# Performance work log

Hardware: AMD Instinct MI355X
Metric: run time of the kernel (lower is better)

The kernel has to match this reference:

```python
import jax, jax.numpy as jnp
import numpy as np

B, N, D = 4, 4096, 1024
HEADS, DIM_HEAD = 16, 64
INNER = HEADS * DIM_HEAD
LN_EPS = 1e-5


def next_fast_len(n):
    # smallest 5-smooth integer >= n (matches scipy.fftpack.next_fast_len)
    while True:
        m = n
        for p in (2, 3, 5):
            while m % p == 0:
                m //= p
        if m == 1:
            return n
        n += 1


def setup_inputs() -> dict:
    key = jax.random.key(0)
    k = jax.random.split(key, 6)
    x = jax.random.normal(k[0], (B, N, D), dtype=jnp.float32)
    gamma = jnp.ones((D,), dtype=jnp.float32)
    beta = jnp.zeros((D,), dtype=jnp.float32)
    alpha = jax.random.normal(k[1], (HEADS,), dtype=jnp.float32)
    w_in = jax.random.normal(k[2], (INNER, D), dtype=jnp.float32) * 0.02
    w_out = jax.random.normal(k[3], (D, INNER), dtype=jnp.float32) * 0.02
    return {"x": x, "gamma": gamma, "beta": beta, "alpha": alpha, "w_in": w_in, "w_out": w_out}


def reference(x, gamma, beta, alpha, w_in, w_out):
    b, n, d = x.shape
    h, dh = HEADS, DIM_HEAD
    # LayerNorm (biased variance, eps=1e-5)
    mu = jnp.mean(x, axis=-1, keepdims=True)
    var = jnp.var(x, axis=-1, keepdims=True)
    xn = (x - mu) * jax.lax.rsqrt(var + LN_EPS) * gamma + beta
    # project_in (no bias), split heads: b n (h d) -> b h n d
    xi = jnp.einsum('bnd,ed->bne', xn, w_in)
    xi = xi.reshape(b, n, h, dh).transpose(0, 2, 1, 3)  # [b,h,n,dh]
    # exponential decay weights per head: alpha * (1-alpha)**flip(arange(n)) -> [h, n]
    a = jax.nn.sigmoid(alpha)[:, None]
    weights = a * (1.0 - a) ** jnp.arange(n - 1, -1, -1, dtype=x.dtype)[None, :]
    # FFT-based causal correlation (conv1d_fft)
    fast_len = next_fast_len(n + n - 1)
    f_x = jnp.fft.rfft(xi, n=fast_len, axis=-2)           # [b,h,L',dh] complex
    f_w = jnp.fft.rfft(weights, n=fast_len, axis=-1)      # [h,L'] complex
    out = jnp.fft.irfft(f_x * jnp.conj(f_w)[None, :, :, None], fast_len, axis=-2)
    out = jnp.roll(out, -1, axis=-2)
    out = out[:, :, fast_len - n:, :]                      # last n positions -> [b,h,n,dh]
    # merge heads and project out
    out = out.transpose(0, 2, 1, 3).reshape(b, n, h * dh)
    return jnp.einsum('bne,de->bnd', out, w_out)
```

## Files before the change

### kernel.cpp

```cpp
#include <hip/hip_runtime.h>
#include <hip/hip_bf16.h>

#define B_ 4
#define N_ 4096
#define D_ 1024
#define H_ 16
#define INNER_ 1024
#define M_ (B_ * N_)
#define CH_ 128
#define CL_ 32

using bf16x8 = __attribute__((ext_vector_type(8))) __bf16;
using f32x4  = __attribute__((ext_vector_type(4))) float;

__device__ __forceinline__ float bf2f(unsigned short v) {
  return __uint_as_float(((unsigned)v) << 16);
}
__device__ __forceinline__ unsigned short f2bf(float f) {
  __hip_bfloat16 h = __float2bfloat16(f);
  return *reinterpret_cast<unsigned short*>(&h);
}
__device__ __forceinline__ float sigm(float x) { return 1.f / (1.f + expf(-x)); }

__device__ __forceinline__ void gload_lds16(const void* g, void* l) {
  __builtin_amdgcn_global_load_lds(
      (const __attribute__((address_space(1))) unsigned int*)g,
      (__attribute__((address_space(3))) unsigned int*)l, 16, 0, 0);
}

__global__ __launch_bounds__(256) void cast_bf16_kernel(
    const float* __restrict__ in, __hip_bfloat16* __restrict__ out, int n4) {
  int i = blockIdx.x * 256 + threadIdx.x;
  if (i >= n4) return;
  float4 v = reinterpret_cast<const float4*>(in)[i];
  ushort4 o;
  o.x = f2bf(v.x); o.y = f2bf(v.y); o.z = f2bf(v.z); o.w = f2bf(v.w);
  reinterpret_cast<ushort4*>(out)[i] = o;
}

__global__ __launch_bounds__(256) void ln_kernel(
    const float* __restrict__ x, const float* __restrict__ gamma,
    const float* __restrict__ beta, __hip_bfloat16* __restrict__ xn) {
  const long row = blockIdx.x;
  const int t = threadIdx.x;
  const float4 v = reinterpret_cast<const float4*>(x + row * D_)[t];
  float s = v.x + v.y + v.z + v.w;
  float s2 = v.x * v.x + v.y * v.y + v.z * v.z + v.w * v.w;
#pragma unroll
  for (int o = 32; o > 0; o >>= 1) {
    s += __shfl_down(s, o);
    s2 += __shfl_down(s2, o);
  }
  __shared__ float red[8];
  const int lane = t & 63, wv = t >> 6;
  if (lane == 0) { red[wv] = s; red[4 + wv] = s2; }
  __syncthreads();
  const float sum = red[0] + red[1] + red[2] + red[3];
  const float sum2 = red[4] + red[5] + red[6] + red[7];
  const float mu = sum * (1.f / D_);
  const float var = sum2 * (1.f / D_) - mu * mu;
  const float rs = rsqrtf(var + 1e-5f);
  const float4 g = reinterpret_cast<const float4*>(gamma)[t];
  const float4 bb = reinterpret_cast<const float4*>(beta)[t];
  ushort4 o;
  o.x = f2bf((v.x - mu) * rs * g.x + bb.x);
  o.y = f2bf((v.y - mu) * rs * g.y + bb.y);
  o.z = f2bf((v.z - mu) * rs * g.z + bb.z);
  o.w = f2bf((v.w - mu) * rs * g.w + bb.w);
  reinterpret_cast<ushort4*>(xn + row * D_)[t] = o;
}

__device__ __forceinline__ void stc(float* p, float v) { *p = v; }
__device__ __forceinline__ void stc(__hip_bfloat16* p, float v) { *p = __float2bfloat16(v); }

template <typename TOUT, int NT>
__global__ __launch_bounds__(512, 2) void gemm256_kernel(
    const __hip_bfloat16* __restrict__ A, const __hip_bfloat16* __restrict__ Bt,
    TOUT* __restrict__ C, int M, int N, int K) {
  static_assert(NT >= 4, "ring needs >=4 tiles");
  __shared__ __align__(16) char lds[131072];
  const int tid = threadIdx.x;
  const int lane = tid & 63;
  const int wave = tid >> 6;

  int wg = blockIdx.y * gridDim.x + blockIdx.x;
  wg = (wg & 7) * 32 + (wg >> 3);
  const int bx = wg & 3;
  const int by = wg >> 2;
  const long bm = (long)by * 256;
  const long bn = (long)bx * 256;

  const int u0  = (tid & 7) ^ ((tid >> 3) & 7);
  const int r0  = 2 * (tid >> 3) + (u0 >> 2);
  const int ck0 = u0 & 3;
  const __hip_bfloat16* sA0 = A  + (bm + r0) * (long)K + ck0 * 8;
  const __hip_bfloat16* sA1 = sA0 + 128l * K;
  const __hip_bfloat16* sB0 = Bt + (bn + r0) * (long)K + ck0 * 8;
  const __hip_bfloat16* sB1 = sB0 + 128l * K;
  char* dbase = (char*)lds + wave * 1024;

  const int wm = wave >> 2;
  const int wn = wave & 3;
  const int fr = lane & 15;
  const int ck = lane >> 4;
  const int pos = (((fr & 1) << 2) | ck) ^ ((fr >> 1) & 7);
  const int laneA = wm * 8192 + (fr >> 1) * 128 + pos * 16;
  const int laneB = 16384 + wn * 4096 + (fr >> 1) * 128 + pos * 16;

  f32x4 acc[8][4] = {};

#define STAGE_A(kt) do { const int _s = (kt) & 3;                         \
    gload_lds16(sA0 + (long)(kt) * 32, dbase + _s * 32768);               \
    gload_lds16(sA1 + (long)(kt) * 32, dbase + _s * 32768 + 8192); } while (0)
#define STAGE_B(kt) do { const int _s = (kt) & 3;                         \
    gload_lds16(sB0 + (long)(kt) * 32, dbase + _s * 32768 + 16384);       \
    gload_lds16(sB1 + (long)(kt) * 32, dbase + _s * 32768 + 24576); } while (0)

  STAGE_A(0); STAGE_B(0);
  STAGE_A(1); STAGE_B(1);
  asm volatile("s_waitcnt vmcnt(4)" ::: "memory");
  __builtin_amdgcn_s_barrier();
  asm volatile("" ::: "memory");

#pragma unroll 4
  for (int t = 0; t < NT; ++t) {
    const char* base = (const char*)lds + (t & 3) * 32768;
    bf16x8 bv[4], av[4];
#pragma unroll
    for (int c = 0; c < 4; ++c) bv[c] = *(const bf16x8*)(base + laneB + c * 1024);
#pragma unroll
    for (int r = 0; r < 4; ++r) av[r] = *(const bf16x8*)(base + laneA + r * 1024);
    if (t + 2 < NT) STAGE_A(t + 2);
    __builtin_amdgcn_s_setprio(1);
#pragma unroll
    for (int r = 0; r < 4; ++r)
#pragma unroll
      for (int c = 0; c < 4; ++c)
        acc[r][c] = __builtin_amdgcn_mfma_f32_16x16x32_bf16(av[r], bv[c], acc[r][c], 0, 0, 0);
    __builtin_amdgcn_s_setprio(0);
#pragma unroll
    for (int r = 0; r < 4; ++r) av[r] = *(const bf16x8*)(base + laneA + (r + 4) * 1024);
    if (t + 2 < NT) STAGE_B(t + 2);
    __builtin_amdgcn_s_setprio(1);
#pragma unroll
    for (int r = 0; r < 4; ++r)
#pragma unroll
      for (int c = 0; c < 4; ++c)
        acc[r + 4][c] = __builtin_amdgcn_mfma_f32_16x16x32_bf16(av[r], bv[c], acc[r + 4][c], 0, 0, 0);
    __builtin_amdgcn_s_setprio(0);
    if (t < NT - 3) asm volatile("s_waitcnt vmcnt(4)" ::: "memory");
    else            asm volatile("s_waitcnt vmcnt(0)" ::: "memory");
    __builtin_amdgcn_s_barrier();
    asm volatile("" ::: "memory");
  }
#undef STAGE_A
#undef STAGE_B

  const int cr = ck * 4;
#pragma unroll
  for (int rf = 0; rf < 8; ++rf)
#pragma unroll
    for (int cf = 0; cf < 4; ++cf)
#pragma unroll
      for (int r = 0; r < 4; ++r) {
        const long row = bm + wm * 128 + rf * 16 + cr + r;
        const long col = bn + wn * 64 + cf * 16 + fr;
        stc(&C[row * (long)N + col], acc[rf][cf][r]);
      }
}

__global__ __launch_bounds__(256) void scan_local_kernel(
    const __hip_bfloat16* __restrict__ xi, __hip_bfloat16* __restrict__ y,
    float* __restrict__ finals, const float* __restrict__ alpha) {
  const int e0 = threadIdx.x * 4;
  const int c = blockIdx.y;
  const int b = blockIdx.z;
  const float a = sigm(alpha[e0 >> 6]);
  const float om = 1.f - a;
  long base = ((long)b * N_ + (long)c * CL_) * INNER_ + e0;
  float y0 = 0.f, y1 = 0.f, y2 = 0.f, y3 = 0.f;
  for (int t = 0; t < CL_; ++t) {
    ushort4 u = *(const ushort4*)(xi + base);
    y0 = om * y0 + a * bf2f(u.x);
    y1 = om * y1 + a * bf2f(u.y);
    y2 = om * y2 + a * bf2f(u.z);
    y3 = om * y3 + a * bf2f(u.w);
    ushort4 o;
    o.x = f2bf(y0); o.y = f2bf(y1); o.z = f2bf(y2); o.w = f2bf(y3);
    *(ushort4*)(y + base) = o;
    base += INNER_;
  }
  float4 f4 = make_float4(y0, y1, y2, y3);
  *reinterpret_cast<float4*>(&finals[((long)b * CH_ + c) * INNER_ + e0]) = f4;
}

__global__ __launch_bounds__(256) void scan_carry_kernel(
    const float* __restrict__ finals, float* __restrict__ carries,
    const float* __restrict__ alpha) {
  const int g = blockIdx.x * 256 + threadIdx.x;
  const int b = g >> 10;
  const int e = g & 1023;
  const float a = sigm(alpha[e >> 6]);
  const float dc = powf(1.f - a, (float)CL_);
  float carry = 0.f;
  for (int c = 0; c < CH_; ++c) {
    const long idx = ((long)b * CH_ + c) * INNER_ + e;
    carries[idx] = carry;
    carry = finals[idx] + dc * carry;
  }
}

__global__ __launch_bounds__(256) void scan_fix_kernel(
    __hip_bfloat16* __restrict__ y, const float* __restrict__ carries,
    const float* __restrict__ alpha) {
  const int t = blockIdx.y;
  const int c = t >> 5;
  if (c == 0) return;
  const int tl = t & 31;
  const int e0 = threadIdx.x * 4;
  const int b = blockIdx.z;
  const float a = sigm(alpha[e0 >> 6]);
  const float om = 1.f - a;
  const float w = exp2f((float)(tl + 1) * log2f(om));
  const float4 cr = *reinterpret_cast<const float4*>(
      &carries[((long)b * CH_ + c) * INNER_ + e0]);
  const long idx = ((long)b * N_ + t) * INNER_ + e0;
  ushort4 u = *(const ushort4*)(y + idx);
  ushort4 o;
  o.x = f2bf(bf2f(u.x) + cr.x * w);
  o.y = f2bf(bf2f(u.y) + cr.y * w);
  o.z = f2bf(bf2f(u.z) + cr.z * w);
  o.w = f2bf(bf2f(u.w) + cr.w * w);
  *(ushort4*)(y + idx) = o;
}

extern "C" void kernel_launch(void* const* d_in, const int* in_sizes, int n_in,
                              void* d_out, int out_size, void* d_ws, size_t ws_size,
                              hipStream_t stream) {
  const float* x     = (const float*)d_in[0];
  const float* gamma = (const float*)d_in[1];
  const float* beta  = (const float*)d_in[2];
  const float* alpha = (const float*)d_in[3];
  const float* w_in  = (const float*)d_in[4];
  const float* w_out = (const float*)d_in[5];
  float* out = (float*)d_out;
  char* ws = (char*)d_ws;

  __hip_bfloat16* xn = (__hip_bfloat16*)ws;
  __hip_bfloat16* wi = (__hip_bfloat16*)(ws + (32l << 20));
  __hip_bfloat16* wo = (__hip_bfloat16*)(ws + (34l << 20));
  float* finals      = (float*)(ws + (36l << 20));
  float* carries     = (float*)(ws + (38l << 20));
  __hip_bfloat16* xi = (__hip_bfloat16*)d_out;

  cast_bf16_kernel<<<1024, 256, 0, stream>>>(w_in, wi, (INNER_ * D_) / 4);
  cast_bf16_kernel<<<1024, 256, 0, stream>>>(w_out, wo, (D_ * INNER_) / 4);

  ln_kernel<<<M_, 256, 0, stream>>>(x, gamma, beta, xn);

  gemm256_kernel<__hip_bfloat16, 32>
      <<<dim3(INNER_ / 256, M_ / 256), 512, 0, stream>>>(xn, wi, xi, M_, INNER_, D_);

  __hip_bfloat16* y = xn;
  scan_local_kernel<<<dim3(1, CH_, B_), 256, 0, stream>>>(xi, y, finals, alpha);
  scan_carry_kernel<<<(B_ * INNER_) / 256, 256, 0, stream>>>(finals, carries, alpha);
  scan_fix_kernel<<<dim3(1, N_, B_), 256, 0, stream>>>(y, carries, alpha);

  gemm256_kernel<float, 32>
      <<<dim3(D_ / 256, M_ / 256), 512, 0, stream>>>(y, wo, out, M_, D_, INNER_);
}
```

Measured before the change: 143.3 us.

## Merge weight casts, restructure scan as finals/apply, add GEMM sub-iteration barriers

Fuses the two weight cast launches into one kernel. The scan becomes reduce-then-rescan: the first pass computes only chunk finals without writing y, and the apply pass recomputes each chunk from its carry and writes y once. This replaces a separate full read-modify-write fix pass with a second read of xi. The GEMM main loop gains extra barriers and sched_barriers around each half-step, uses a separate register set for the second A fragment, and adjusts the vmcnt waits. The added barriers may cost more than the scheduling control saves.

```diff
diff --git a/kernel.cpp b/kernel.cpp
--- a/kernel.cpp
+++ b/kernel.cpp
@@ -28,14 +28,18 @@
       (__attribute__((address_space(3))) unsigned int*)l, 16, 0, 0);
 }
 
-__global__ __launch_bounds__(256) void cast_bf16_kernel(
-    const float* __restrict__ in, __hip_bfloat16* __restrict__ out, int n4) {
+#define W4_ ((INNER_ * D_) / 4)
+__global__ __launch_bounds__(256) void cast2_kernel(
+    const float* __restrict__ wa, const float* __restrict__ wb,
+    __hip_bfloat16* __restrict__ oa, __hip_bfloat16* __restrict__ ob) {
   int i = blockIdx.x * 256 + threadIdx.x;
-  if (i >= n4) return;
-  float4 v = reinterpret_cast<const float4*>(in)[i];
+  const float* src = (i < W4_) ? wa : wb;
+  __hip_bfloat16* dst = (i < W4_) ? oa : ob;
+  int j = (i < W4_) ? i : i - W4_;
+  float4 v = reinterpret_cast<const float4*>(src)[j];
   ushort4 o;
   o.x = f2bf(v.x); o.y = f2bf(v.y); o.z = f2bf(v.z); o.w = f2bf(v.w);
-  reinterpret_cast<ushort4*>(out)[i] = o;
+  reinterpret_cast<ushort4*>(dst)[j] = o;
 }
 
 __global__ __launch_bounds__(256) void ln_kernel(
@@ -115,22 +119,27 @@
 #define STAGE_B(kt) do { const int _s = (kt) & 3;                         \
     gload_lds16(sB0 + (long)(kt) * 32, dbase + _s * 32768 + 16384);       \
     gload_lds16(sB1 + (long)(kt) * 32, dbase + _s * 32768 + 24576); } while (0)
+#define SBAR() asm volatile("s_barrier" ::: "memory")
+#define SCHED0() __builtin_amdgcn_sched_barrier(0)
 
   STAGE_A(0); STAGE_B(0);
   STAGE_A(1); STAGE_B(1);
   asm volatile("s_waitcnt vmcnt(4)" ::: "memory");
-  __builtin_amdgcn_s_barrier();
-  asm volatile("" ::: "memory");
+  SBAR();
 
 #pragma unroll 4
   for (int t = 0; t < NT; ++t) {
     const char* base = (const char*)lds + (t & 3) * 32768;
-    bf16x8 bv[4], av[4];
+    bf16x8 bv[4], av[4], av2[4];
 #pragma unroll
     for (int c = 0; c < 4; ++c) bv[c] = *(const bf16x8*)(base + laneB + c * 1024);
 #pragma unroll
     for (int r = 0; r < 4; ++r) av[r] = *(const bf16x8*)(base + laneA + r * 1024);
     if (t + 2 < NT) STAGE_A(t + 2);
+    SCHED0();
+    SBAR();
+    asm volatile("s_waitcnt lgkmcnt(0)" ::: "memory");
+    SCHED0();
     __builtin_amdgcn_s_setprio(1);
 #pragma unroll
     for (int r = 0; r < 4; ++r)
@@ -138,23 +147,31 @@
       for (int c = 0; c < 4; ++c)
         acc[r][c] = __builtin_amdgcn_mfma_f32_16x16x32_bf16(av[r], bv[c], acc[r][c], 0, 0, 0);
     __builtin_amdgcn_s_setprio(0);
-#pragma unroll
-    for (int r = 0; r < 4; ++r) av[r] = *(const bf16x8*)(base + laneA + (r + 4) * 1024);
+    SCHED0();
+    SBAR();
+#pragma unroll
+    for (int r = 0; r < 4; ++r) av2[r] = *(const bf16x8*)(base + laneA + (r + 4) * 1024);
     if (t + 2 < NT) STAGE_B(t + 2);
+    SCHED0();
+    SBAR();
+    asm volatile("s_waitcnt lgkmcnt(0)" ::: "memory");
+    SCHED0();
     __builtin_amdgcn_s_setprio(1);
 #pragma unroll
     for (int r = 0; r < 4; ++r)
 #pragma unroll
       for (int c = 0; c < 4; ++c)
-        acc[r + 4][c] = __builtin_amdgcn_mfma_f32_16x16x32_bf16(av[r], bv[c], acc[r + 4][c], 0, 0, 0);
+        acc[r + 4][c] = __builtin_amdgcn_mfma_f32_16x16x32_bf16(av2[r], bv[c], acc[r + 4][c], 0, 0, 0);
     __builtin_amdgcn_s_setprio(0);
-    if (t < NT - 3) asm volatile("s_waitcnt vmcnt(4)" ::: "memory");
-    else            asm volatile("s_waitcnt vmcnt(0)" ::: "memory");
-    __builtin_amdgcn_s_barrier();
-    asm volatile("" ::: "memory");
+    SCHED0();
+    if (t < NT - 2)       asm volatile("s_waitcnt vmcnt(4)" ::: "memory");
+    else if (t == NT - 2) asm volatile("s_waitcnt vmcnt(0)" ::: "memory");
+    SBAR();
   }
 #undef STAGE_A
 #undef STAGE_B
+#undef SBAR
+#undef SCHED0
 
   const int cr = ck * 4;
 #pragma unroll
@@ -169,9 +186,9 @@
       }
 }
 
-__global__ __launch_bounds__(256) void scan_local_kernel(
-    const __hip_bfloat16* __restrict__ xi, __hip_bfloat16* __restrict__ y,
-    float* __restrict__ finals, const float* __restrict__ alpha) {
+__global__ __launch_bounds__(256) void scan_finals_kernel(
+    const __hip_bfloat16* __restrict__ xi, float* __restrict__ finals,
+    const float* __restrict__ alpha) {
   const int e0 = threadIdx.x * 4;
   const int c = blockIdx.y;
   const int b = blockIdx.z;
@@ -185,9 +202,6 @@
     y1 = om * y1 + a * bf2f(u.y);
     y2 = om * y2 + a * bf2f(u.z);
     y3 = om * y3 + a * bf2f(u.w);
-    ushort4 o;
-    o.x = f2bf(y0); o.y = f2bf(y1); o.z = f2bf(y2); o.w = f2bf(y3);
-    *(ushort4*)(y + base) = o;
     base += INNER_;
   }
   float4 f4 = make_float4(y0, y1, y2, y3);
@@ -210,28 +224,29 @@
   }
 }
 
-__global__ __launch_bounds__(256) void scan_fix_kernel(
-    __hip_bfloat16* __restrict__ y, const float* __restrict__ carries,
-    const float* __restrict__ alpha) {
-  const int t = blockIdx.y;
-  const int c = t >> 5;
-  if (c == 0) return;
-  const int tl = t & 31;
+__global__ __launch_bounds__(256) void scan_apply_kernel(
+    const __hip_bfloat16* __restrict__ xi, __hip_bfloat16* __restrict__ y,
+    const float* __restrict__ carries, const float* __restrict__ alpha) {
   const int e0 = threadIdx.x * 4;
+  const int c = blockIdx.y;
   const int b = blockIdx.z;
   const float a = sigm(alpha[e0 >> 6]);
   const float om = 1.f - a;
-  const float w = exp2f((float)(tl + 1) * log2f(om));
   const float4 cr = *reinterpret_cast<const float4*>(
       &carries[((long)b * CH_ + c) * INNER_ + e0]);
-  const long idx = ((long)b * N_ + t) * INNER_ + e0;
-  ushort4 u = *(const ushort4*)(y + idx);
-  ushort4 o;
-  o.x = f2bf(bf2f(u.x) + cr.x * w);
-  o.y = f2bf(bf2f(u.y) + cr.y * w);
-  o.z = f2bf(bf2f(u.z) + cr.z * w);
-  o.w = f2bf(bf2f(u.w) + cr.w * w);
-  *(ushort4*)(y + idx) = o;
+  float y0 = cr.x, y1 = cr.y, y2 = cr.z, y3 = cr.w;
+  long base = ((long)b * N_ + (long)c * CL_) * INNER_ + e0;
+  for (int t = 0; t < CL_; ++t) {
+    ushort4 u = *(const ushort4*)(xi + base);
+    y0 = om * y0 + a * bf2f(u.x);
+    y1 = om * y1 + a * bf2f(u.y);
+    y2 = om * y2 + a * bf2f(u.z);
+    y3 = om * y3 + a * bf2f(u.w);
+    ushort4 o;
+    o.x = f2bf(y0); o.y = f2bf(y1); o.z = f2bf(y2); o.w = f2bf(y3);
+    *(ushort4*)(y + base) = o;
+    base += INNER_;
+  }
 }
 
 extern "C" void kernel_launch(void* const* d_in, const int* in_sizes, int n_in,
@@ -253,8 +268,7 @@
   float* carries     = (float*)(ws + (38l << 20));
   __hip_bfloat16* xi = (__hip_bfloat16*)d_out;
 
-  cast_bf16_kernel<<<1024, 256, 0, stream>>>(w_in, wi, (INNER_ * D_) / 4);
-  cast_bf16_kernel<<<1024, 256, 0, stream>>>(w_out, wo, (D_ * INNER_) / 4);
+  cast2_kernel<<<2048, 256, 0, stream>>>(w_in, w_out, wi, wo);
 
   ln_kernel<<<M_, 256, 0, stream>>>(x, gamma, beta, xn);
 
@@ -262,9 +276,9 @@
       <<<dim3(INNER_ / 256, M_ / 256), 512, 0, stream>>>(xn, wi, xi, M_, INNER_, D_);
 
   __hip_bfloat16* y = xn;
-  scan_local_kernel<<<dim3(1, CH_, B_), 256, 0, stream>>>(xi, y, finals, alpha);
+  scan_finals_kernel<<<dim3(1, CH_, B_), 256, 0, stream>>>(xi, finals, alpha);
   scan_carry_kernel<<<(B_ * INNER_) / 256, 256, 0, stream>>>(finals, carries, alpha);
-  scan_fix_kernel<<<dim3(1, N_, B_), 256, 0, stream>>>(y, carries, alpha);
+  scan_apply_kernel<<<dim3(1, CH_, B_), 256, 0, stream>>>(xi, y, carries, alpha);
 
   gemm256_kernel<float, 32>
       <<<dim3(D_ / 256, M_ / 256), 512, 0, stream>>>(y, wo, out, M_, D_, INNER_);
```

Result: faster. 132.9 us (-7.3%).
